# Performance work log

Measured on AMD Instinct MI355X. Metric: run time of the kernel, lower is better.

Reference implementation:

```python
import jax, jax.numpy as jnp
import numpy as np

N = [50000, 150000, 100000, 40000, 10000]  # cells per rank 0..4
C = 64       # channels (all ranks, in == out)
DEG = 8      # avg adjacency degree
INC = 4      # avg incidence nnz per higher-rank cell
PAIRS = [(0, 1), (1, 2), (2, 3), (3, 4)]


def _xavier(key, shape):
    s = float(np.sqrt(6.0 / (shape[0] + shape[1])))
    return jax.random.uniform(key, shape, jnp.float32, -s, s)


def setup_inputs() -> dict:
    key = jax.random.key(0)
    ks = iter(jax.random.split(key, 100))
    inp = {}
    for r in range(5):
        inp[f"x_{r}"] = jax.random.normal(next(ks), (N[r], C), jnp.float32)
        nnz = DEG * N[r]
        inp[f"a{r}_r"] = jax.random.randint(next(ks), (nnz,), 0, N[r], jnp.int32)
        inp[f"a{r}_c"] = jax.random.randint(next(ks), (nnz,), 0, N[r], jnp.int32)
        inp[f"a{r}_v"] = jax.random.uniform(next(ks), (nnz,), jnp.float32)
        inp[f"cci_{r}"] = jax.random.uniform(next(ks), (N[r], C), jnp.float32)
        inp[f"W_hbs_{r}"] = _xavier(next(ks), (C, C))
        inp[f"W_agg_{r}"] = _xavier(next(ks), (C, C))
    for a, b in PAIRS:
        nnz = INC * N[b]
        inp[f"i{a}{b}_t"] = jax.random.randint(next(ks), (nnz,), 0, N[a], jnp.int32)
        inp[f"i{a}{b}_s"] = jax.random.randint(next(ks), (nnz,), 0, N[b], jnp.int32)
        inp[f"i{a}{b}_v"] = jax.random.uniform(next(ks), (nnz,), jnp.float32)
        inp[f"W_s{a}{b}"] = _xavier(next(ks), (C, C))
        inp[f"W_t{a}{b}"] = _xavier(next(ks), (C, C))
    return inp


def _spmm(rows, cols, vals, x, n_out):
    # COO sparse matmul: out[i] = sum over entries e with rows[e]==i of vals[e]*x[cols[e]]
    return jax.ops.segment_sum(vals[:, None] * x[cols], rows, num_segments=n_out)


def _forward(x, av, cci, Wh, iv, Ws, Wt, Wg, ar, ac, it, isrc):
    relu = jax.nn.relu
    # HBS per rank: x_r_to_r = relu(cci_r * (A_r @ (x_r @ W_r)))
    same = [relu(cci[r] * _spmm(ar[r], ac[r], av[r], x[r] @ Wh[r], N[r])) for r in range(5)]
    down = {}  # message from rank b to rank a via incidence B_{a,b}
    up = {}    # message from rank a to rank b via B_{a,b}^T
    for k, (a, b) in enumerate(PAIRS):
        down[(b, a)] = relu(_spmm(it[k], isrc[k], iv[k], x[b] @ Ws[k], N[a]))
        up[(a, b)] = relu(_spmm(isrc[k], it[k], iv[k], x[a] @ Wt[k], N[b]))
    # RankAggregator: relu(sum(messages) @ W_agg)
    out0 = relu((same[0] + down[(1, 0)]) @ Wg[0])
    out1 = relu((up[(0, 1)] + same[1] + down[(2, 1)]) @ Wg[1])
    out2 = relu((up[(1, 2)] + same[2] + down[(3, 2)]) @ Wg[2])
    out3 = relu((up[(2, 3)] + same[3] + down[(4, 3)]) @ Wg[3])
    out4 = relu((up[(3, 4)] + same[4]) @ Wg[4])
    return (out0, out1, out2, out3, out4)


def reference(x_0, x_1, x_2, x_3, x_4,
              a0_r, a0_c, a0_v, a1_r, a1_c, a1_v, a2_r, a2_c, a2_v,
              a3_r, a3_c, a3_v, a4_r, a4_c, a4_v,
              cci_0, cci_1, cci_2, cci_3, cci_4,
              W_hbs_0, W_hbs_1, W_hbs_2, W_hbs_3, W_hbs_4,
              W_agg_0, W_agg_1, W_agg_2, W_agg_3, W_agg_4,
              i01_t, i01_s, i01_v, i12_t, i12_s, i12_v,
              i23_t, i23_s, i23_v, i34_t, i34_s, i34_v,
              W_s01, W_t01, W_s12, W_t12, W_s23, W_t23, W_s34, W_t34):
    return _forward([x_0, x_1, x_2, x_3, x_4],
                    [a0_v, a1_v, a2_v, a3_v, a4_v],
                    [cci_0, cci_1, cci_2, cci_3, cci_4],
                    [W_hbs_0, W_hbs_1, W_hbs_2, W_hbs_3, W_hbs_4],
                    [i01_v, i12_v, i23_v, i34_v],
                    [W_s01, W_s12, W_s23, W_s34],
                    [W_t01, W_t12, W_t23, W_t34],
                    [W_agg_0, W_agg_1, W_agg_2, W_agg_3, W_agg_4],
                    [a0_r, a1_r, a2_r, a3_r, a4_r],
                    [a0_c, a1_c, a2_c, a3_c, a4_c],
                    [i01_t, i12_t, i23_t, i34_t],
                    [i01_s, i12_s, i23_s, i34_s])
```

## Files before the change

### kernel.cpp

```cpp
#include <hip/hip_runtime.h>
#include <hip/hip_bf16.h>

__device__ __forceinline__ float bf2f(unsigned short u) {
    union { unsigned int i; float f; } v;
    v.i = ((unsigned int)u) << 16;
    return v.f;
}
__device__ __forceinline__ unsigned short f2bf(float f) {
    __hip_bfloat16 h = __float2bfloat16(f);
    return *reinterpret_cast<unsigned short*>(&h);
}
__device__ __forceinline__ int xc(int r, int c) { return c ^ ((r & 3) << 3); }

__global__ void probe_dtype(const unsigned short* __restrict__ x, int* flag) {
    if (blockIdx.x == 0 && threadIdx.x == 0) {
        int wild = 0;
        for (int i = 0; i < 512; ++i) {
            unsigned e = (x[i] >> 7) & 0xFF;
            if (e >= 0xC0) ++wild;
        }
        *flag = (wild > 0) ? 1 : 0;
    }
}

struct Seg {
    const int*  rows;
    const int*  cols;
    const void* vals;
    int*  cnt;
    int*  rp;
    int*  bsum;
    uint2* ed;
    int nnz;
    int n;
};
struct Seg3 { Seg s[3]; };

__global__ __launch_bounds__(256) void hist_all(Seg3 B) {
    Seg S = B.s[blockIdx.y];
    int e = blockIdx.x * 256 + threadIdx.x;
    if (e < S.nnz) atomicAdd(&S.cnt[S.rows[e]], 1);
}

__global__ __launch_bounds__(256) void scan1_all(Seg3 B) {
    Seg S = B.s[blockIdx.y];
    __shared__ int sm[256];
    const int t = threadIdx.x;
    const int base = blockIdx.x * 1024 + t * 4;
    int v[4]; int sum = 0;
#pragma unroll
    for (int j = 0; j < 4; ++j) { int i = base + j; v[j] = (i < S.n) ? S.cnt[i] : 0; sum += v[j]; }
    sm[t] = sum; __syncthreads();
    for (int off = 1; off < 256; off <<= 1) {
        int xv = (t >= off) ? sm[t - off] : 0;
        __syncthreads();
        sm[t] += xv;
        __syncthreads();
    }
    int run = sm[t] - sum;
#pragma unroll
    for (int j = 0; j < 4; ++j) { int i = base + j; if (i < S.n) S.rp[i] = run; run += v[j]; }
    if (t == 255) S.bsum[blockIdx.x] = sm[255];
}

__global__ __launch_bounds__(256) void scan2_all(Seg3 B) {
    Seg S = B.s[blockIdx.y];
    __shared__ int red[256];
    const int t = threadIdx.x;
    const int g0 = blockIdx.x >> 2;
    int v = (t < g0) ? S.bsum[t] : 0;
    red[t] = v; __syncthreads();
    for (int o = 128; o; o >>= 1) { if (t < o) red[t] += red[t + o]; __syncthreads(); }
    int i = blockIdx.x * 256 + t;
    if (i < S.n) S.rp[i] += red[0];
}

__global__ __launch_bounds__(256) void fill_all(Seg3 B, const int* __restrict__ flag) {
    Seg S = B.s[blockIdx.y];
    int e = blockIdx.x * 256 + threadIdx.x;
    if (e >= S.nnz) return;
    int r = S.rows[e];
    int pos = atomicAdd(&S.rp[r], 1);
    float v = (*flag) ? ((const float*)S.vals)[e]
                      : bf2f(((const unsigned short*)S.vals)[e]);
    uint2 ed; ed.x = (unsigned)S.cols[e]; ed.y = __float_as_uint(v);
    S.ed[pos] = ed;
}

template<int FL>
__device__ __forceinline__ void gather16(
    const int* __restrict__ rp, const uint2* __restrict__ ed,
    const void* __restrict__ x, float xsh[64][64],
    int row0, int nrows, int wv, int lane)
{
    const int rbase = row0 + wv * 16;
    int rv = 0;
    {
        int t = rbase - 1 + lane;
        if (lane <= 16 && t >= 0 && t < nrows) rv = rp[t];
    }
    for (int i = 0; i < 16; ++i) {
        int row = rbase + i;
        int e0 = __shfl(rv, i, 64);
        int e1 = __shfl(rv, i + 1, 64);
        float acc = 0.f;
        if (row < nrows) {
            for (int e = e0; e < e1; e += 8) {
                uint2 d[8];
#pragma unroll
                for (int j = 0; j < 8; ++j) {
                    int idx = e + j;
                    idx = (idx < e1) ? idx : (e1 - 1);
                    d[j] = ed[idx];
                }
                float xv[8];
#pragma unroll
                for (int j = 0; j < 8; ++j) {
                    size_t off = (size_t)d[j].x * 64 + lane;
                    xv[j] = FL ? ((const float*)x)[off]
                               : bf2f(((const unsigned short*)x)[off]);
                }
#pragma unroll
                for (int j = 0; j < 8; ++j) {
                    float v = (e + j < e1) ? __uint_as_float(d[j].y) : 0.f;
                    acc = fmaf(v, xv[j], acc);
                }
            }
        }
        xsh[wv * 16 + i][xc(wv * 16 + i, lane)] = acc;
    }
}

struct RankArgs {
    const int*   rp[3];
    const uint2* ed[3];
    const void*  xsrc[3];
    const void*  W[3];
    const void*  cci;
    const void*  Wg;
    long long    mbase;
    int          nrows;
    int          nph;
};

__global__ __launch_bounds__(256, 4) void rank_fused(
    RankArgs A, void* __restrict__ dout, const int* __restrict__ flag)
{
    __shared__ float Ws[64][64];
    __shared__ float xsh[64][64];
    const int tid = threadIdx.x;
    const int fl = *flag;
    const int row0 = blockIdx.x * 64;
    const int wv   = __builtin_amdgcn_readfirstlane(tid >> 6);
    const int lane = tid & 63;
    const int tx = tid & 15, ty = tid >> 4;

    float C[4][4];
#pragma unroll
    for (int a = 0; a < 4; ++a)
#pragma unroll
        for (int b = 0; b < 4; ++b) C[a][b] = 0.f;

    for (int p = 0; p < A.nph; ++p) {
        __syncthreads();
        if (fl) {
            const float* Wf = (const float*)A.W[p];
            for (int i = tid; i < 4096; i += 256) Ws[i >> 6][i & 63] = Wf[i];
        } else {
            const unsigned short* Wb = (const unsigned short*)A.W[p];
            for (int i = tid; i < 4096; i += 256) Ws[i >> 6][i & 63] = bf2f(Wb[i]);
        }
        if (fl) gather16<1>(A.rp[p], A.ed[p], A.xsrc[p], xsh, row0, A.nrows, wv, lane);
        else    gather16<0>(A.rp[p], A.ed[p], A.xsrc[p], xsh, row0, A.nrows, wv, lane);
        __syncthreads();

        float a4[4][4];
#pragma unroll
        for (int a = 0; a < 4; ++a)
#pragma unroll
            for (int b = 0; b < 4; ++b) a4[a][b] = 0.f;

#pragma unroll 8
        for (int k = 0; k < 64; ++k) {
            float4 w4 = *reinterpret_cast<const float4*>(&Ws[k][tx << 2]);
#pragma unroll
            for (int rr = 0; rr < 4; ++rr) {
                int r = ty + 16 * rr;
                float xv = xsh[r][xc(r, k)];
                a4[rr][0] += xv * w4.x;
                a4[rr][1] += xv * w4.y;
                a4[rr][2] += xv * w4.z;
                a4[rr][3] += xv * w4.w;
            }
        }

        if (p == 0) {
#pragma unroll
            for (int rr = 0; rr < 4; ++rr) {
                int l = row0 + ty + 16 * rr;
                if (l >= A.nrows) continue;
                size_t co = (size_t)l * 64 + (tx << 2);
                float c4[4];
                if (fl) {
                    float4 cv = *reinterpret_cast<const float4*>(&((const float*)A.cci)[co]);
                    c4[0] = cv.x; c4[1] = cv.y; c4[2] = cv.z; c4[3] = cv.w;
                } else {
                    ushort4 cv = *reinterpret_cast<const ushort4*>(&((const unsigned short*)A.cci)[co]);
                    c4[0] = bf2f(cv.x); c4[1] = bf2f(cv.y); c4[2] = bf2f(cv.z); c4[3] = bf2f(cv.w);
                }
#pragma unroll
                for (int j = 0; j < 4; ++j) C[rr][j] += fmaxf(a4[rr][j] * c4[j], 0.f);
            }
        } else {
#pragma unroll
            for (int rr = 0; rr < 4; ++rr)
#pragma unroll
                for (int j = 0; j < 4; ++j) C[rr][j] += fmaxf(a4[rr][j], 0.f);
        }
    }

    __syncthreads();
#pragma unroll
    for (int rr = 0; rr < 4; ++rr) {
        int r = ty + 16 * rr;
#pragma unroll
        for (int j = 0; j < 4; ++j) xsh[r][xc(r, (tx << 2) + j)] = C[rr][j];
    }
    if (fl) {
        const float* Wf = (const float*)A.Wg;
        for (int i = tid; i < 4096; i += 256) Ws[i >> 6][i & 63] = Wf[i];
    } else {
        const unsigned short* Wb = (const unsigned short*)A.Wg;
        for (int i = tid; i < 4096; i += 256) Ws[i >> 6][i & 63] = bf2f(Wb[i]);
    }
    __syncthreads();

    float a4[4][4];
#pragma unroll
    for (int a = 0; a < 4; ++a)
#pragma unroll
        for (int b = 0; b < 4; ++b) a4[a][b] = 0.f;
#pragma unroll 8
    for (int k = 0; k < 64; ++k) {
        float4 w4 = *reinterpret_cast<const float4*>(&Ws[k][tx << 2]);
#pragma unroll
        for (int rr = 0; rr < 4; ++rr) {
            int r = ty + 16 * rr;
            float xv = xsh[r][xc(r, k)];
            a4[rr][0] += xv * w4.x;
            a4[rr][1] += xv * w4.y;
            a4[rr][2] += xv * w4.z;
            a4[rr][3] += xv * w4.w;
        }
    }
#pragma unroll
    for (int rr = 0; rr < 4; ++rr) {
        int l = row0 + ty + 16 * rr;
        if (l >= A.nrows) continue;
        size_t ob = (size_t)A.mbase + (size_t)l * 64 + (tx << 2);
        if (fl) {
            float4 o;
            o.x = fmaxf(a4[rr][0], 0.f); o.y = fmaxf(a4[rr][1], 0.f);
            o.z = fmaxf(a4[rr][2], 0.f); o.w = fmaxf(a4[rr][3], 0.f);
            *reinterpret_cast<float4*>(&((float*)dout)[ob]) = o;
        } else {
            ushort4 o;
            o.x = f2bf(fmaxf(a4[rr][0], 0.f)); o.y = f2bf(fmaxf(a4[rr][1], 0.f));
            o.z = f2bf(fmaxf(a4[rr][2], 0.f)); o.w = f2bf(fmaxf(a4[rr][3], 0.f));
            *reinterpret_cast<ushort4*>(&((unsigned short*)dout)[ob]) = o;
        }
    }
}

__global__ __launch_bounds__(256, 4) void spmm_gemm(
    const int* __restrict__ rp, const uint2* __restrict__ edges,
    const void* __restrict__ x, const void* __restrict__ W,
    const void* __restrict__ cci, void* mout, const int* __restrict__ flag,
    int nrows, long long mbase, int mode)
{
    __shared__ float Ws[64][64];
    __shared__ float xsh[64][64];
    const int tid = threadIdx.x;
    const int fl = *flag;
    const int row0 = blockIdx.x * 64;
    const int wv   = __builtin_amdgcn_readfirstlane(tid >> 6);
    const int lane = tid & 63;

    if (fl) {
        const float* Wf = (const float*)W;
        for (int i = tid; i < 4096; i += 256) Ws[i >> 6][i & 63] = Wf[i];
    } else {
        const unsigned short* Wb = (const unsigned short*)W;
        for (int i = tid; i < 4096; i += 256) Ws[i >> 6][i & 63] = bf2f(Wb[i]);
    }
    if (fl) gather16<1>(rp, edges, x, xsh, row0, nrows, wv, lane);
    else    gather16<0>(rp, edges, x, xsh, row0, nrows, wv, lane);
    __syncthreads();

    const int tx = tid & 15, ty = tid >> 4;
    float a4[4][4];
#pragma unroll
    for (int a = 0; a < 4; ++a)
#pragma unroll
        for (int b = 0; b < 4; ++b) a4[a][b] = 0.f;

#pragma unroll 8
    for (int k = 0; k < 64; ++k) {
        float4 w4 = *reinterpret_cast<const float4*>(&Ws[k][tx << 2]);
#pragma unroll
        for (int rr = 0; rr < 4; ++rr) {
            int r = ty + 16 * rr;
            float xv = xsh[r][xc(r, k)];
            a4[rr][0] += xv * w4.x;
            a4[rr][1] += xv * w4.y;
            a4[rr][2] += xv * w4.z;
            a4[rr][3] += xv * w4.w;
        }
    }

#pragma unroll
    for (int rr = 0; rr < 4; ++rr) {
        int l = row0 + ty + 16 * rr;
        if (l >= nrows) continue;
        size_t co = (size_t)l * 64 + (tx << 2);
        size_t ob = (size_t)mbase + co;
        float t[4] = { a4[rr][0], a4[rr][1], a4[rr][2], a4[rr][3] };
        if (mode == 0) {
            float c4[4];
            if (fl) {
                float4 cv = *reinterpret_cast<const float4*>(&((const float*)cci)[co]);
                c4[0] = cv.x; c4[1] = cv.y; c4[2] = cv.z; c4[3] = cv.w;
            } else {
                ushort4 cv = *reinterpret_cast<const ushort4*>(&((const unsigned short*)cci)[co]);
                c4[0] = bf2f(cv.x); c4[1] = bf2f(cv.y); c4[2] = bf2f(cv.z); c4[3] = bf2f(cv.w);
            }
#pragma unroll
            for (int j = 0; j < 4; ++j) t[j] = fmaxf(t[j] * c4[j], 0.f);
            if (fl) {
                float4 o; o.x = t[0]; o.y = t[1]; o.z = t[2]; o.w = t[3];
                *reinterpret_cast<float4*>(&((float*)mout)[ob]) = o;
            } else {
                ushort4 o; o.x = f2bf(t[0]); o.y = f2bf(t[1]); o.z = f2bf(t[2]); o.w = f2bf(t[3]);
                *reinterpret_cast<ushort4*>(&((unsigned short*)mout)[ob]) = o;
            }
        } else {
            if (fl) {
                float* mp = (float*)mout;
                float4 ov = *reinterpret_cast<const float4*>(&mp[ob]);
                float4 o;
                o.x = ov.x + fmaxf(t[0], 0.f);
                o.y = ov.y + fmaxf(t[1], 0.f);
                o.z = ov.z + fmaxf(t[2], 0.f);
                o.w = ov.w + fmaxf(t[3], 0.f);
                *reinterpret_cast<float4*>(&mp[ob]) = o;
            } else {
                unsigned short* mp = (unsigned short*)mout;
                ushort4 ov = *reinterpret_cast<const ushort4*>(&mp[ob]);
                ushort4 o;
                o.x = f2bf(bf2f(ov.x) + fmaxf(t[0], 0.f));
                o.y = f2bf(bf2f(ov.y) + fmaxf(t[1], 0.f));
                o.z = f2bf(bf2f(ov.z) + fmaxf(t[2], 0.f));
                o.w = f2bf(bf2f(ov.w) + fmaxf(t[3], 0.f));
                *reinterpret_cast<ushort4*>(&mp[ob]) = o;
            }
        }
    }
}

__global__ __launch_bounds__(256) void finalize(
    void* mout, const void* __restrict__ Wg, const int* __restrict__ flag,
    int N, long long mbase)
{
    __shared__ float Ws[64][64];
    __shared__ float ms[64][65];
    const int tid = threadIdx.x;
    const int tx = tid & 15, ty = tid >> 4;
    const int fl = *flag;

    if (fl) {
        const float* Wf = (const float*)Wg;
        for (int i = tid; i < 4096; i += 256) Ws[i >> 6][i & 63] = Wf[i];
    } else {
        const unsigned short* Wb = (const unsigned short*)Wg;
        for (int i = tid; i < 4096; i += 256) Ws[i >> 6][i & 63] = bf2f(Wb[i]);
    }
    const int row0 = blockIdx.x * 64;
    for (int i = tid; i < 4096; i += 256) {
        int r = i >> 6, c = i & 63;
        int g = row0 + r;
        float v = 0.f;
        if (g < N) {
            size_t o = (size_t)mbase + (size_t)g * 64 + c;
            v = fl ? ((const float*)mout)[o] : bf2f(((const unsigned short*)mout)[o]);
        }
        ms[r][c] = v;
    }
    __syncthreads();

    float a4[4][4];
#pragma unroll
    for (int a = 0; a < 4; ++a)
#pragma unroll
        for (int b = 0; b < 4; ++b) a4[a][b] = 0.f;

#pragma unroll 8
    for (int k = 0; k < 64; ++k) {
        float4 w4 = *reinterpret_cast<const float4*>(&Ws[k][tx << 2]);
#pragma unroll
        for (int rr = 0; rr < 4; ++rr) {
            float xv = ms[ty + 16 * rr][k];
            a4[rr][0] += xv * w4.x;
            a4[rr][1] += xv * w4.y;
            a4[rr][2] += xv * w4.z;
            a4[rr][3] += xv * w4.w;
        }
    }
#pragma unroll
    for (int rr = 0; rr < 4; ++rr) {
        int g = row0 + ty + 16 * rr;
        if (g >= N) continue;
        size_t ob = (size_t)mbase + (size_t)g * 64 + (tx << 2);
        if (fl) {
            float4 o;
            o.x = fmaxf(a4[rr][0], 0.f); o.y = fmaxf(a4[rr][1], 0.f);
            o.z = fmaxf(a4[rr][2], 0.f); o.w = fmaxf(a4[rr][3], 0.f);
            *reinterpret_cast<float4*>(&((float*)mout)[ob]) = o;
        } else {
            ushort4 o;
            o.x = f2bf(fmaxf(a4[rr][0], 0.f)); o.y = f2bf(fmaxf(a4[rr][1], 0.f));
            o.z = f2bf(fmaxf(a4[rr][2], 0.f)); o.w = f2bf(fmaxf(a4[rr][3], 0.f));
            *reinterpret_cast<ushort4*>(&((unsigned short*)mout)[ob]) = o;
        }
    }
}

__global__ __launch_bounds__(256) void scatter_x(
    const int* __restrict__ rows, const int* __restrict__ cols,
    const void* __restrict__ vals, const void* __restrict__ x,
    const int* __restrict__ flag,
    float* __restrict__ acc, int nnz, int r0, int r1)
{
    int e = blockIdx.x * 4 + threadIdx.y;
    if (e >= nnz) return;
    int r = rows[e];
    if (r < r0 || r >= r1) return;
    int c = threadIdx.x;
    int cc = cols[e];
    const int fl = *flag;
    float v, xv;
    if (fl) {
        v  = ((const float*)vals)[e];
        xv = ((const float*)x)[(size_t)cc * 64 + c];
    } else {
        v  = bf2f(((const unsigned short*)vals)[e]);
        xv = bf2f(((const unsigned short*)x)[(size_t)cc * 64 + c]);
    }
    atomicAdd(&acc[(size_t)(r - r0) * 64 + c], v * xv);
}

__global__ __launch_bounds__(256) void gemm_phase(
    const float* __restrict__ acc,
    const void* __restrict__ W,
    const void* __restrict__ cci,
    void* mout,
    const int* __restrict__ flag,
    int n_rows, long long grow0, long long mbase, int mode)
{
    __shared__ float Ws[64][64];
    __shared__ float xs[64][65];
    const int tid = threadIdx.x;
    const int tx = tid & 15, ty = tid >> 4;
    const int fl = *flag;

    if (fl) {
        const float* Wf = (const float*)W;
        for (int i = tid; i < 4096; i += 256) Ws[i >> 6][i & 63] = Wf[i];
    } else {
        const unsigned short* Wb = (const unsigned short*)W;
        for (int i = tid; i < 4096; i += 256) Ws[i >> 6][i & 63] = bf2f(Wb[i]);
    }
    const int lrow0 = blockIdx.x * 64;
    for (int i = tid; i < 4096; i += 256) {
        int r = i >> 6, c = i & 63;
        int l = lrow0 + r;
        xs[r][c] = (l < n_rows) ? acc[(size_t)l * 64 + c] : 0.f;
    }
    __syncthreads();

    float a4[4][4];
#pragma unroll
    for (int a = 0; a < 4; ++a)
#pragma unroll
        for (int b = 0; b < 4; ++b) a4[a][b] = 0.f;

#pragma unroll 8
    for (int k = 0; k < 64; ++k) {
        float4 w4 = *reinterpret_cast<const float4*>(&Ws[k][tx << 2]);
#pragma unroll
        for (int rr = 0; rr < 4; ++rr) {
            float xv = xs[ty + 16 * rr][k];
            a4[rr][0] += xv * w4.x;
            a4[rr][1] += xv * w4.y;
            a4[rr][2] += xv * w4.z;
            a4[rr][3] += xv * w4.w;
        }
    }

#pragma unroll
    for (int rr = 0; rr < 4; ++rr) {
        int l = lrow0 + ty + 16 * rr;
        if (l >= n_rows) continue;
        long long g = grow0 + l;
        size_t co = (size_t)g * 64 + (tx << 2);
        size_t ob = (size_t)mbase + co;
        float t[4] = { a4[rr][0], a4[rr][1], a4[rr][2], a4[rr][3] };
        if (mode == 0) {
            float c4[4];
            if (fl) {
                float4 cv = *reinterpret_cast<const float4*>(&((const float*)cci)[co]);
                c4[0] = cv.x; c4[1] = cv.y; c4[2] = cv.z; c4[3] = cv.w;
            } else {
                ushort4 cv = *reinterpret_cast<const ushort4*>(&((const unsigned short*)cci)[co]);
                c4[0] = bf2f(cv.x); c4[1] = bf2f(cv.y); c4[2] = bf2f(cv.z); c4[3] = bf2f(cv.w);
            }
#pragma unroll
            for (int j = 0; j < 4; ++j) t[j] = fmaxf(t[j] * c4[j], 0.f);
            if (fl) {
                float4 o; o.x = t[0]; o.y = t[1]; o.z = t[2]; o.w = t[3];
                *reinterpret_cast<float4*>(&((float*)mout)[ob]) = o;
            } else {
                ushort4 o; o.x = f2bf(t[0]); o.y = f2bf(t[1]); o.z = f2bf(t[2]); o.w = f2bf(t[3]);
                *reinterpret_cast<ushort4*>(&((unsigned short*)mout)[ob]) = o;
            }
        } else {
            if (fl) {
                float* mp = (float*)mout;
                float4 ov = *reinterpret_cast<const float4*>(&mp[ob]);
                float4 o;
                o.x = ov.x + fmaxf(t[0], 0.f);
                o.y = ov.y + fmaxf(t[1], 0.f);
                o.z = ov.z + fmaxf(t[2], 0.f);
                o.w = ov.w + fmaxf(t[3], 0.f);
                *reinterpret_cast<float4*>(&mp[ob]) = o;
            } else {
                unsigned short* mp = (unsigned short*)mout;
                ushort4 ov = *reinterpret_cast<const ushort4*>(&mp[ob]);
                ushort4 o;
                o.x = f2bf(bf2f(ov.x) + fmaxf(t[0], 0.f));
                o.y = f2bf(bf2f(ov.y) + fmaxf(t[1], 0.f));
                o.z = f2bf(bf2f(ov.z) + fmaxf(t[2], 0.f));
                o.w = f2bf(bf2f(ov.w) + fmaxf(t[3], 0.f));
                *reinterpret_cast<ushort4*>(&mp[ob]) = o;
            }
        }
    }
}

extern "C" void kernel_launch(void* const* d_in, const int* in_sizes, int n_in,
                              void* d_out, int out_size, void* d_ws, size_t ws_size,
                              hipStream_t stream)
{
    static const int Ns[5] = {50000, 150000, 100000, 40000, 10000};

    const void *x[5], *av[5], *cci[5], *Whbs[5], *Wagg[5];
    const int *ar[5], *ac[5];
    int nnzA[5];
    for (int r = 0; r < 5; ++r) {
        x[r]    = d_in[r * 7 + 0];
        ar[r]   = (const int*)d_in[r * 7 + 1];
        ac[r]   = (const int*)d_in[r * 7 + 2];
        av[r]   = d_in[r * 7 + 3];
        cci[r]  = d_in[r * 7 + 4];
        Whbs[r] = d_in[r * 7 + 5];
        Wagg[r] = d_in[r * 7 + 6];
        nnzA[r] = in_sizes[r * 7 + 3];
    }
    const int *it[4], *is[4];
    const void *iv[4], *Wsp[4], *Wtp[4];
    int nnzI[4];
    for (int k = 0; k < 4; ++k) {
        it[k]  = (const int*)d_in[35 + k * 5 + 0];
        is[k]  = (const int*)d_in[35 + k * 5 + 1];
        iv[k]  = d_in[35 + k * 5 + 2];
        Wsp[k] = d_in[35 + k * 5 + 3];
        Wtp[k] = d_in[35 + k * 5 + 4];
        nnzI[k] = in_sizes[35 + k * 5 + 2];
    }

    char* ws = (char*)d_ws;
    size_t flag_off = (ws_size >= 4096) ? ((ws_size - 4) & ~(size_t)3) : 0;
    int* flag = (int*)(ws + flag_off);

    probe_dtype<<<1, 64, 0, stream>>>((const unsigned short*)x[0], flag);

    auto al16 = [](size_t v) { return (v + 15) & ~(size_t)15; };
    dim3 b256(256);
    long long base = 0;

    for (int r = 0; r < 5; ++r) {
        const int N = Ns[r];

        struct Ph { const int* rw; const int* cl; const void* vl; const void* xs;
                    const void* W; int nnz; };
        Ph ph[3]; int np = 0;
        ph[np++] = { ar[r], ac[r], av[r], x[r], Whbs[r], nnzA[r] };
        if (r < 4) ph[np++] = { it[r], is[r], iv[r], x[r + 1], Wsp[r], nnzI[r] };
        if (r > 0) ph[np++] = { is[r-1], it[r-1], iv[r-1], x[r - 1], Wtp[r-1], nnzI[r-1] };

        size_t cntOff = 0;
        size_t rpOff  = al16((size_t)np * N * 4);
        size_t bsOff  = rpOff + al16((size_t)np * N * 4);
        size_t edOff  = al16(bsOff + (size_t)np * 256 * 4);
        size_t edSz = 0;
        for (int p = 0; p < np; ++p) edSz += al16((size_t)ph[p].nnz * 8);
        size_t need = edOff + edSz;

        if (need + 64 <= flag_off) {
            Seg3 B{};
            size_t ep = edOff;
            int maxnnz = 0;
            for (int p = 0; p < np; ++p) {
                B.s[p].rows = ph[p].rw;  B.s[p].cols = ph[p].cl;  B.s[p].vals = ph[p].vl;
                B.s[p].cnt  = (int*)(ws + cntOff) + (size_t)p * N;
                B.s[p].rp   = (int*)(ws + rpOff)  + (size_t)p * N;
                B.s[p].bsum = (int*)(ws + bsOff)  + (size_t)p * 256;
                B.s[p].ed   = (uint2*)(ws + ep);
                B.s[p].nnz  = ph[p].nnz;
                B.s[p].n    = N;
                ep += al16((size_t)ph[p].nnz * 8);
                if (ph[p].nnz > maxnnz) maxnnz = ph[p].nnz;
            }
            hipMemsetAsync(ws + cntOff, 0, (size_t)np * N * 4, stream);
            hist_all <<<dim3((maxnnz + 255) / 256, np), b256, 0, stream>>>(B);
            scan1_all<<<dim3((N + 1023) / 1024, np), b256, 0, stream>>>(B);
            scan2_all<<<dim3((N + 255) / 256, np), b256, 0, stream>>>(B);
            fill_all <<<dim3((maxnnz + 255) / 256, np), b256, 0, stream>>>(B, flag);

            RankArgs A{};
            for (int p = 0; p < np; ++p) {
                A.rp[p]   = B.s[p].rp;
                A.ed[p]   = B.s[p].ed;
                A.xsrc[p] = ph[p].xs;
                A.W[p]    = ph[p].W;
            }
            A.cci = cci[r]; A.Wg = Wagg[r];
            A.mbase = base; A.nrows = N; A.nph = np;
            rank_fused<<<(N + 63) / 64, b256, 0, stream>>>(A, d_out, flag);
        } else {
            for (int p = 0; p < np; ++p) {
                const int nnz = ph[p].nnz;
                size_t cOff = 0;
                size_t rOff = al16((size_t)N * 4);
                size_t bOff = rOff + al16((size_t)N * 4);
                size_t eOff = al16(bOff + 1024);
                size_t need3 = eOff + (size_t)nnz * 8;
                if (need3 + 64 <= flag_off) {
                    Seg3 B{};
                    B.s[0].rows = ph[p].rw; B.s[0].cols = ph[p].cl; B.s[0].vals = ph[p].vl;
                    B.s[0].cnt  = (int*)(ws + cOff);
                    B.s[0].rp   = (int*)(ws + rOff);
                    B.s[0].bsum = (int*)(ws + bOff);
                    B.s[0].ed   = (uint2*)(ws + eOff);
                    B.s[0].nnz  = nnz; B.s[0].n = N;
                    hipMemsetAsync(ws + cOff, 0, (size_t)N * 4, stream);
                    hist_all <<<dim3((nnz + 255) / 256, 1), b256, 0, stream>>>(B);
                    scan1_all<<<dim3((N + 1023) / 1024, 1), b256, 0, stream>>>(B);
                    scan2_all<<<dim3((N + 255) / 256, 1), b256, 0, stream>>>(B);
                    fill_all <<<dim3((nnz + 255) / 256, 1), b256, 0, stream>>>(B, flag);
                    spmm_gemm<<<(N + 63) / 64, b256, 0, stream>>>(
                        B.s[0].rp, B.s[0].ed, ph[p].xs, ph[p].W, cci[r], d_out, flag,
                        N, base, (p == 0) ? 0 : 1);
                } else {
                    long long budget = (flag_off > 256) ? (long long)((flag_off - 256) / 256) : 64;
                    budget &= ~63LL;
                    if (budget < 64) budget = 64;
                    float* acc = (float*)ws;
                    dim3 sb(64, 4);
                    for (long long r0 = 0; r0 < N; r0 += budget) {
                        int rc = (int)((N - r0 < budget) ? (N - r0) : budget);
                        hipMemsetAsync(acc, 0, (size_t)rc * 256, stream);
                        scatter_x<<<(nnz + 3) / 4, sb, 0, stream>>>(
                            ph[p].rw, ph[p].cl, ph[p].vl, ph[p].xs, flag,
                            acc, nnz, (int)r0, (int)(r0 + rc));
                        gemm_phase<<<(rc + 63) / 64, b256, 0, stream>>>(
                            acc, ph[p].W, cci[r], d_out, flag,
                            rc, r0, base, (p == 0) ? 0 : 1);
                    }
                }
            }
            finalize<<<(N + 63) / 64, b256, 0, stream>>>(d_out, Wagg[r], flag, N, base);
        }
        base += (long long)N * 64;
    }
}
```

Baseline: 1.555 ms.

## Batch CSR construction for all ranks into one launch set and template rank kernel

Builds the CSR structures for all 13 sparse operators in a single memset plus one launch each of hist/scan1/scan2/fill, instead of repeating those launches per rank. Each rank's fused kernel then runs without the CSR kernels interleaved between ranks. rank_fused is templated on the phase count so the phase loop can unroll, and the gather uses readlane with precomputed byte offsets. The cost is a larger workspace requirement and grids sized to the largest segment, so blocks for smaller segments launch and exit with no work.

```diff
diff --git a/kernel.cpp b/kernel.cpp
--- a/kernel.cpp
+++ b/kernel.cpp
@@ -34,16 +34,26 @@
     int nnz;
     int n;
 };
-struct Seg3 { Seg s[3]; };
-
-__global__ __launch_bounds__(256) void hist_all(Seg3 B) {
-    Seg S = B.s[blockIdx.y];
+struct SegArr { Seg s[13]; };
+
+__device__ __forceinline__ Seg pick(const SegArr& B, int y) {
+    switch (y) {
+        case 0: return B.s[0];  case 1: return B.s[1];  case 2: return B.s[2];
+        case 3: return B.s[3];  case 4: return B.s[4];  case 5: return B.s[5];
+        case 6: return B.s[6];  case 7: return B.s[7];  case 8: return B.s[8];
+        case 9: return B.s[9];  case 10: return B.s[10]; case 11: return B.s[11];
+        default: return B.s[12];
+    }
+}
+
+__global__ __launch_bounds__(256) void hist_all(SegArr B) {
+    Seg S = pick(B, blockIdx.y);
     int e = blockIdx.x * 256 + threadIdx.x;
     if (e < S.nnz) atomicAdd(&S.cnt[S.rows[e]], 1);
 }
 
-__global__ __launch_bounds__(256) void scan1_all(Seg3 B) {
-    Seg S = B.s[blockIdx.y];
+__global__ __launch_bounds__(256) void scan1_all(SegArr B) {
+    Seg S = pick(B, blockIdx.y);
     __shared__ int sm[256];
     const int t = threadIdx.x;
     const int base = blockIdx.x * 1024 + t * 4;
@@ -63,8 +73,8 @@
     if (t == 255) S.bsum[blockIdx.x] = sm[255];
 }
 
-__global__ __launch_bounds__(256) void scan2_all(Seg3 B) {
-    Seg S = B.s[blockIdx.y];
+__global__ __launch_bounds__(256) void scan2_all(SegArr B) {
+    Seg S = pick(B, blockIdx.y);
     __shared__ int red[256];
     const int t = threadIdx.x;
     const int g0 = blockIdx.x >> 2;
@@ -75,8 +85,8 @@
     if (i < S.n) S.rp[i] += red[0];
 }
 
-__global__ __launch_bounds__(256) void fill_all(Seg3 B, const int* __restrict__ flag) {
-    Seg S = B.s[blockIdx.y];
+__global__ __launch_bounds__(256) void fill_all(SegArr B, const int* __restrict__ flag) {
+    Seg S = pick(B, blockIdx.y);
     int e = blockIdx.x * 256 + threadIdx.x;
     if (e >= S.nnz) return;
     int r = S.rows[e];
@@ -99,35 +109,33 @@
         int t = rbase - 1 + lane;
         if (lane <= 16 && t >= 0 && t < nrows) rv = rp[t];
     }
+    const int lb = lane * (FL ? 4 : 2);
     for (int i = 0; i < 16; ++i) {
         int row = rbase + i;
-        int e0 = __shfl(rv, i, 64);
-        int e1 = __shfl(rv, i + 1, 64);
+        int e0 = __builtin_amdgcn_readlane(rv, i);
+        int e1 = __builtin_amdgcn_readlane(rv, i + 1);
         float acc = 0.f;
         if (row < nrows) {
             for (int e = e0; e < e1; e += 8) {
-                uint2 d[8];
+                const char* xb[8]; float vv[8];
 #pragma unroll
                 for (int j = 0; j < 8; ++j) {
-                    int idx = e + j;
-                    idx = (idx < e1) ? idx : (e1 - 1);
-                    d[j] = ed[idx];
+                    int idx = (e + j < e1) ? (e + j) : (e1 - 1);
+                    uint2 d = ed[idx];
+                    xb[j] = (const char*)x + (size_t)(d.x * (unsigned)(FL ? 256 : 128));
+                    vv[j] = (e + j < e1) ? __uint_as_float(d.y) : 0.f;
                 }
                 float xv[8];
 #pragma unroll
-                for (int j = 0; j < 8; ++j) {
-                    size_t off = (size_t)d[j].x * 64 + lane;
-                    xv[j] = FL ? ((const float*)x)[off]
-                               : bf2f(((const unsigned short*)x)[off]);
-                }
-#pragma unroll
-                for (int j = 0; j < 8; ++j) {
-                    float v = (e + j < e1) ? __uint_as_float(d[j].y) : 0.f;
-                    acc = fmaf(v, xv[j], acc);
-                }
-            }
-        }
-        xsh[wv * 16 + i][xc(wv * 16 + i, lane)] = acc;
+                for (int j = 0; j < 8; ++j)
+                    xv[j] = FL ? *(const float*)(xb[j] + lb)
+                               : bf2f(*(const unsigned short*)(xb[j] + lb));
+#pragma unroll
+                for (int j = 0; j < 8; ++j) acc = fmaf(vv[j], xv[j], acc);
+            }
+        }
+        int lr = wv * 16 + i;
+        xsh[lr][xc(lr, lane)] = acc;
     }
 }
 
@@ -140,9 +148,9 @@
     const void*  Wg;
     long long    mbase;
     int          nrows;
-    int          nph;
 };
 
+template<int NPH>
 __global__ __launch_bounds__(256, 4) void rank_fused(
     RankArgs A, void* __restrict__ dout, const int* __restrict__ flag)
 {
@@ -161,7 +169,8 @@
 #pragma unroll
         for (int b = 0; b < 4; ++b) C[a][b] = 0.f;
 
-    for (int p = 0; p < A.nph; ++p) {
+#pragma unroll
+    for (int p = 0; p < NPH; ++p) {
         __syncthreads();
         if (fl) {
             const float* Wf = (const float*)A.W[p];
@@ -595,101 +604,161 @@
 
     auto al16 = [](size_t v) { return (v + 15) & ~(size_t)15; };
     dim3 b256(256);
-    long long base = 0;
+
+    struct Ph { const int* rw; const int* cl; const void* vl; const void* xs;
+                const void* W; int nnz; int n; };
+    Ph P[13]; int seg0[5], npr[5]; int NP = 0;
+    for (int r = 0; r < 5; ++r) {
+        seg0[r] = NP;
+        P[NP++] = { ar[r], ac[r], av[r], x[r], Whbs[r], nnzA[r], Ns[r] };
+        if (r < 4) P[NP++] = { it[r], is[r], iv[r], x[r + 1], Wsp[r], nnzI[r], Ns[r] };
+        if (r > 0) P[NP++] = { is[r-1], it[r-1], iv[r-1], x[r - 1], Wtp[r-1], nnzI[r-1], Ns[r] };
+        npr[r] = NP - seg0[r];
+    }
+    long long mb[5]; { long long b = 0; for (int r = 0; r < 5; ++r) { mb[r] = b; b += (long long)Ns[r] * 64; } }
+
+    long long sumN = 0; int maxN = 0, maxnnz = 0;
+    for (int i = 0; i < NP; ++i) {
+        sumN += P[i].n;
+        if (P[i].n > maxN) maxN = P[i].n;
+        if (P[i].nnz > maxnnz) maxnnz = P[i].nnz;
+    }
+    size_t cntOff = 0;
+    size_t rpOff  = al16((size_t)sumN * 4);
+    size_t bsOff  = rpOff + al16((size_t)sumN * 4);
+    size_t edOff0 = bsOff + al16((size_t)NP * 256 * 4);
+    size_t edSz = 0;
+    for (int i = 0; i < NP; ++i) edSz += al16((size_t)P[i].nnz * 8);
+    size_t needA = edOff0 + edSz;
+
+    if (needA + 64 <= flag_off) {
+        SegArr SA{};
+        size_t ep = edOff0; long long cum = 0;
+        for (int i = 0; i < NP; ++i) {
+            SA.s[i].rows = P[i].rw; SA.s[i].cols = P[i].cl; SA.s[i].vals = P[i].vl;
+            SA.s[i].cnt  = (int*)(ws + cntOff) + cum;
+            SA.s[i].rp   = (int*)(ws + rpOff)  + cum;
+            SA.s[i].bsum = (int*)(ws + bsOff)  + (size_t)i * 256;
+            SA.s[i].ed   = (uint2*)(ws + ep);
+            SA.s[i].nnz  = P[i].nnz;
+            SA.s[i].n    = P[i].n;
+            cum += P[i].n;
+            ep += al16((size_t)P[i].nnz * 8);
+        }
+        hipMemsetAsync(ws + cntOff, 0, (size_t)sumN * 4, stream);
+        hist_all <<<dim3((maxnnz + 255) / 256, NP), b256, 0, stream>>>(SA);
+        scan1_all<<<dim3((maxN + 1023) / 1024, NP), b256, 0, stream>>>(SA);
+        scan2_all<<<dim3((maxN + 255) / 256, NP), b256, 0, stream>>>(SA);
+        fill_all <<<dim3((maxnnz + 255) / 256, NP), b256, 0, stream>>>(SA, flag);
+
+        for (int r = 0; r < 5; ++r) {
+            RankArgs A{};
+            for (int p = 0; p < npr[r]; ++p) {
+                int i = seg0[r] + p;
+                A.rp[p]   = SA.s[i].rp;
+                A.ed[p]   = SA.s[i].ed;
+                A.xsrc[p] = P[i].xs;
+                A.W[p]    = P[i].W;
+            }
+            A.cci = cci[r]; A.Wg = Wagg[r];
+            A.mbase = mb[r]; A.nrows = Ns[r];
+            int grid = (Ns[r] + 63) / 64;
+            if (npr[r] == 3) rank_fused<3><<<grid, b256, 0, stream>>>(A, d_out, flag);
+            else             rank_fused<2><<<grid, b256, 0, stream>>>(A, d_out, flag);
+        }
+        return;
+    }
 
     for (int r = 0; r < 5; ++r) {
         const int N = Ns[r];
-
-        struct Ph { const int* rw; const int* cl; const void* vl; const void* xs;
-                    const void* W; int nnz; };
-        Ph ph[3]; int np = 0;
-        ph[np++] = { ar[r], ac[r], av[r], x[r], Whbs[r], nnzA[r] };
-        if (r < 4) ph[np++] = { it[r], is[r], iv[r], x[r + 1], Wsp[r], nnzI[r] };
-        if (r > 0) ph[np++] = { is[r-1], it[r-1], iv[r-1], x[r - 1], Wtp[r-1], nnzI[r-1] };
-
-        size_t cntOff = 0;
-        size_t rpOff  = al16((size_t)np * N * 4);
-        size_t bsOff  = rpOff + al16((size_t)np * N * 4);
-        size_t edOff  = al16(bsOff + (size_t)np * 256 * 4);
-        size_t edSz = 0;
-        for (int p = 0; p < np; ++p) edSz += al16((size_t)ph[p].nnz * 8);
-        size_t need = edOff + edSz;
-
-        if (need + 64 <= flag_off) {
-            Seg3 B{};
-            size_t ep = edOff;
-            int maxnnz = 0;
+        const int np = npr[r];
+        size_t cOff = 0;
+        size_t rOff = al16((size_t)np * N * 4);
+        size_t bOff = rOff + al16((size_t)np * N * 4);
+        size_t eOff = bOff + al16((size_t)np * 256 * 4);
+        size_t eSz = 0;
+        for (int p = 0; p < np; ++p) eSz += al16((size_t)P[seg0[r] + p].nnz * 8);
+        size_t needB = eOff + eSz;
+
+        if (needB + 64 <= flag_off) {
+            SegArr SB{};
+            size_t ep = eOff;
+            int mxz = 0;
             for (int p = 0; p < np; ++p) {
-                B.s[p].rows = ph[p].rw;  B.s[p].cols = ph[p].cl;  B.s[p].vals = ph[p].vl;
-                B.s[p].cnt  = (int*)(ws + cntOff) + (size_t)p * N;
-                B.s[p].rp   = (int*)(ws + rpOff)  + (size_t)p * N;
-                B.s[p].bsum = (int*)(ws + bsOff)  + (size_t)p * 256;
-                B.s[p].ed   = (uint2*)(ws + ep);
-                B.s[p].nnz  = ph[p].nnz;
-                B.s[p].n    = N;
-                ep += al16((size_t)ph[p].nnz * 8);
-                if (ph[p].nnz > maxnnz) maxnnz = ph[p].nnz;
-            }
-            hipMemsetAsync(ws + cntOff, 0, (size_t)np * N * 4, stream);
-            hist_all <<<dim3((maxnnz + 255) / 256, np), b256, 0, stream>>>(B);
-            scan1_all<<<dim3((N + 1023) / 1024, np), b256, 0, stream>>>(B);
-            scan2_all<<<dim3((N + 255) / 256, np), b256, 0, stream>>>(B);
-            fill_all <<<dim3((maxnnz + 255) / 256, np), b256, 0, stream>>>(B, flag);
+                const Ph& q = P[seg0[r] + p];
+                SB.s[p].rows = q.rw; SB.s[p].cols = q.cl; SB.s[p].vals = q.vl;
+                SB.s[p].cnt  = (int*)(ws + cOff) + (size_t)p * N;
+                SB.s[p].rp   = (int*)(ws + rOff) + (size_t)p * N;
+                SB.s[p].bsum = (int*)(ws + bOff) + (size_t)p * 256;
+                SB.s[p].ed   = (uint2*)(ws + ep);
+                SB.s[p].nnz  = q.nnz;
+                SB.s[p].n    = N;
+                ep += al16((size_t)q.nnz * 8);
+                if (q.nnz > mxz) mxz = q.nnz;
+            }
+            hipMemsetAsync(ws + cOff, 0, (size_t)np * N * 4, stream);
+            hist_all <<<dim3((mxz + 255) / 256, np), b256, 0, stream>>>(SB);
+            scan1_all<<<dim3((N + 1023) / 1024, np), b256, 0, stream>>>(SB);
+            scan2_all<<<dim3((N + 255) / 256, np), b256, 0, stream>>>(SB);
+            fill_all <<<dim3((mxz + 255) / 256, np), b256, 0, stream>>>(SB, flag);
 
             RankArgs A{};
             for (int p = 0; p < np; ++p) {
-                A.rp[p]   = B.s[p].rp;
-                A.ed[p]   = B.s[p].ed;
-                A.xsrc[p] = ph[p].xs;
-                A.W[p]    = ph[p].W;
+                A.rp[p]   = SB.s[p].rp;
+                A.ed[p]   = SB.s[p].ed;
+                A.xsrc[p] = P[seg0[r] + p].xs;
+                A.W[p]    = P[seg0[r] + p].W;
             }
             A.cci = cci[r]; A.Wg = Wagg[r];
-            A.mbase = base; A.nrows = N; A.nph = np;
-            rank_fused<<<(N + 63) / 64, b256, 0, stream>>>(A, d_out, flag);
-        } else {
-            for (int p = 0; p < np; ++p) {
-                const int nnz = ph[p].nnz;
-                size_t cOff = 0;
-                size_t rOff = al16((size_t)N * 4);
-                size_t bOff = rOff + al16((size_t)N * 4);
-                size_t eOff = al16(bOff + 1024);
-                size_t need3 = eOff + (size_t)nnz * 8;
-                if (need3 + 64 <= flag_off) {
-                    Seg3 B{};
-                    B.s[0].rows = ph[p].rw; B.s[0].cols = ph[p].cl; B.s[0].vals = ph[p].vl;
-                    B.s[0].cnt  = (int*)(ws + cOff);
-                    B.s[0].rp   = (int*)(ws + rOff);
-                    B.s[0].bsum = (int*)(ws + bOff);
-                    B.s[0].ed   = (uint2*)(ws + eOff);
-                    B.s[0].nnz  = nnz; B.s[0].n = N;
-                    hipMemsetAsync(ws + cOff, 0, (size_t)N * 4, stream);
-                    hist_all <<<dim3((nnz + 255) / 256, 1), b256, 0, stream>>>(B);
-                    scan1_all<<<dim3((N + 1023) / 1024, 1), b256, 0, stream>>>(B);
-                    scan2_all<<<dim3((N + 255) / 256, 1), b256, 0, stream>>>(B);
-                    fill_all <<<dim3((nnz + 255) / 256, 1), b256, 0, stream>>>(B, flag);
-                    spmm_gemm<<<(N + 63) / 64, b256, 0, stream>>>(
-                        B.s[0].rp, B.s[0].ed, ph[p].xs, ph[p].W, cci[r], d_out, flag,
-                        N, base, (p == 0) ? 0 : 1);
-                } else {
-                    long long budget = (flag_off > 256) ? (long long)((flag_off - 256) / 256) : 64;
-                    budget &= ~63LL;
-                    if (budget < 64) budget = 64;
-                    float* acc = (float*)ws;
-                    dim3 sb(64, 4);
-                    for (long long r0 = 0; r0 < N; r0 += budget) {
-                        int rc = (int)((N - r0 < budget) ? (N - r0) : budget);
-                        hipMemsetAsync(acc, 0, (size_t)rc * 256, stream);
-                        scatter_x<<<(nnz + 3) / 4, sb, 0, stream>>>(
-                            ph[p].rw, ph[p].cl, ph[p].vl, ph[p].xs, flag,
-                            acc, nnz, (int)r0, (int)(r0 + rc));
-                        gemm_phase<<<(rc + 63) / 64, b256, 0, stream>>>(
-                            acc, ph[p].W, cci[r], d_out, flag,
-                            rc, r0, base, (p == 0) ? 0 : 1);
-                    }
+            A.mbase = mb[r]; A.nrows = N;
+            int grid = (N + 63) / 64;
+            if (np == 3) rank_fused<3><<<grid, b256, 0, stream>>>(A, d_out, flag);
+            else         rank_fused<2><<<grid, b256, 0, stream>>>(A, d_out, flag);
+            continue;
+        }
+
+        for (int p = 0; p < np; ++p) {
+            const Ph& q = P[seg0[r] + p];
+            const int nnz = q.nnz;
+            size_t c3 = 0;
+            size_t r3 = al16((size_t)N * 4);
+            size_t b3 = r3 + al16((size_t)N * 4);
+            size_t e3 = b3 + al16(1024);
+            size_t need3 = e3 + (size_t)nnz * 8;
+            if (need3 + 64 <= flag_off) {
+                SegArr SC{};
+                SC.s[0].rows = q.rw; SC.s[0].cols = q.cl; SC.s[0].vals = q.vl;
+                SC.s[0].cnt  = (int*)(ws + c3);
+                SC.s[0].rp   = (int*)(ws + r3);
+                SC.s[0].bsum = (int*)(ws + b3);
+                SC.s[0].ed   = (uint2*)(ws + e3);
+                SC.s[0].nnz  = nnz; SC.s[0].n = N;
+                hipMemsetAsync(ws + c3, 0, (size_t)N * 4, stream);
+                hist_all <<<dim3((nnz + 255) / 256, 1), b256, 0, stream>>>(SC);
+                scan1_all<<<dim3((N + 1023) / 1024, 1), b256, 0, stream>>>(SC);
+                scan2_all<<<dim3((N + 255) / 256, 1), b256, 0, stream>>>(SC);
+                fill_all <<<dim3((nnz + 255) / 256, 1), b256, 0, stream>>>(SC, flag);
+                spmm_gemm<<<(N + 63) / 64, b256, 0, stream>>>(
+                    SC.s[0].rp, SC.s[0].ed, q.xs, q.W, cci[r], d_out, flag,
+                    N, mb[r], (p == 0) ? 0 : 1);
+            } else {
+                long long budget = (flag_off > 256) ? (long long)((flag_off - 256) / 256) : 64;
+                budget &= ~63LL;
+                if (budget < 64) budget = 64;
+                float* acc = (float*)ws;
+                dim3 sb(64, 4);
+                for (long long r0 = 0; r0 < N; r0 += budget) {
+                    int rc = (int)((N - r0 < budget) ? (N - r0) : budget);
+                    hipMemsetAsync(acc, 0, (size_t)rc * 256, stream);
+                    scatter_x<<<(nnz + 3) / 4, sb, 0, stream>>>(
+                        q.rw, q.cl, q.vl, q.xs, flag,
+                        acc, nnz, (int)r0, (int)(r0 + rc));
+                    gemm_phase<<<(rc + 63) / 64, b256, 0, stream>>>(
+                        acc, q.W, cci[r], d_out, flag,
+                        rc, r0, mb[r], (p == 0) ? 0 : 1);
                 }
             }
-            finalize<<<(N + 63) / 64, b256, 0, stream>>>(d_out, Wagg[r], flag, N, base);
-        }
-        base += (long long)N * 64;
-    }
-}
+        }
+        finalize<<<(N + 63) / 64, b256, 0, stream>>>(d_out, Wagg[r], flag, N, mb[r]);
+    }
+}
```

Result: faster. 1.475 ms (-5.2%).
